# Optimization experiments

Measured on AMD Instinct MI355X. Metric: run time of the kernel, lower is better.

## Reference

```python
import jax, jax.numpy as jnp
import numpy as np

N_EMBD = 1024
HEAD_SIZE = 64
N_HEADS = 16
BLOCK_SIZE = 2048


def setup_inputs() -> dict:
    key = jax.random.key(0)
    ks = jax.random.split(key, 7)
    s = 0.02
    return {
        "X": jax.random.normal(ks[0], (2, BLOCK_SIZE, N_EMBD), dtype=jnp.float32),
        # per-head projection weights, torch Linear layout [out, in] stacked over heads
        "Wq": jax.random.normal(ks[1], (N_HEADS, HEAD_SIZE, N_EMBD), dtype=jnp.float32) * s,
        "Wk": jax.random.normal(ks[2], (N_HEADS, HEAD_SIZE, N_EMBD), dtype=jnp.float32) * s,
        "Wv": jax.random.normal(ks[3], (N_HEADS, HEAD_SIZE, N_EMBD), dtype=jnp.float32) * s,
        "Wp": jax.random.normal(ks[4], (N_EMBD, N_EMBD), dtype=jnp.float32) * s,
        "bp": jax.random.normal(ks[5], (N_EMBD,), dtype=jnp.float32) * s,
    }


def reference(X, Wq, Wk, Wv, Wp, bp):
    B, T, C = X.shape
    # per-head projections: [B,H,T,D]
    q = jnp.einsum("btc,hdc->bhtd", X, Wq)
    k = jnp.einsum("btc,hdc->bhtd", X, Wk)
    v = jnp.einsum("btc,hdc->bhtd", X, Wv)
    # NOTE: original scales by C**-0.5 where C = n_embd (not head_size)
    scores = jnp.einsum("bhtd,bhsd->bhts", q, k) * (C ** -0.5)  # [B,H,T,T]
    causal = jnp.tril(jnp.ones((T, T), dtype=bool))
    scores = jnp.where(causal, scores, -jnp.inf)
    weights = jax.nn.softmax(scores, axis=-1)
    out = jnp.einsum("bhts,bhsd->bhtd", weights, v)  # [B,H,T,D]
    # concat heads along last dim: [B,T,H*D]
    out = out.transpose(0, 2, 1, 3).reshape(B, T, -1)
    # output projection (dropout is identity in eval)
    return out @ Wp.T + bp
```

## Files before the change

kernel.cpp:

```cpp
#include <hip/hip_runtime.h>
#include <hip/hip_bf16.h>

typedef __bf16 bf16_t;
typedef __bf16 bf16x8 __attribute__((ext_vector_type(8)));
typedef __bf16 bf16x4 __attribute__((ext_vector_type(4)));
typedef float  f32x4  __attribute__((ext_vector_type(4)));
typedef unsigned int u32x4 __attribute__((ext_vector_type(4)));

#define MFMA16(a,b,c) __builtin_amdgcn_mfma_f32_16x16x32_bf16(a,b,c,0,0,0)

constexpr int B_ = 2, T_ = 2048, H_ = 16, D_ = 64, C_ = 1024;
constexpr int GK = C_;

typedef const __attribute__((address_space(1))) unsigned char ga_t;
typedef __attribute__((address_space(3))) unsigned char la_t;
__device__ __forceinline__ void gld16(const void* g, void* l) {
  __builtin_amdgcn_global_load_lds((ga_t*)g, (la_t*)l, 16, 0, 0);
}

__global__ __launch_bounds__(256) void cast_all(
    const float* __restrict__ X,  const float* __restrict__ Wq,
    const float* __restrict__ Wk, const float* __restrict__ Wv,
    const float* __restrict__ Wp,
    bf16_t* __restrict__ Xb,  bf16_t* __restrict__ Wqb, bf16_t* __restrict__ Wkb,
    bf16_t* __restrict__ Wvb, bf16_t* __restrict__ Wpb)
{
  int i = blockIdx.x * 256 + threadIdx.x;
  const float* src; bf16_t* dst; int off;
  if      (i < 1048576) { src = X;  dst = Xb;  off = i; }
  else if (i < 1310720) { src = Wq; dst = Wqb; off = i - 1048576; }
  else if (i < 1572864) { src = Wk; dst = Wkb; off = i - 1310720; }
  else if (i < 1835008) { src = Wv; dst = Wvb; off = i - 1572864; }
  else                  { src = Wp; dst = Wpb; off = i - 1835008; }
  float4 v = *reinterpret_cast<const float4*>(src + (size_t)off * 4);
  bf16x4 o;
  o[0] = (bf16_t)v.x; o[1] = (bf16_t)v.y; o[2] = (bf16_t)v.z; o[3] = (bf16_t)v.w;
  *reinterpret_cast<bf16x4*>(dst + (size_t)off * 4) = o;
}

__device__ __forceinline__ void gemm128_core(
    const bf16_t* __restrict__ A, const bf16_t* __restrict__ Bw,
    bf16_t* sA, bf16_t* sB, f32x4 (&acc)[4][2], int bx, int by)
{
  const int tid = threadIdx.x, lane = tid & 63, wid = tid >> 6;
  const int wm = wid >> 2, wn = wid & 3;
  const int g = lane >> 4, c = lane & 15, rk = c & 7;
  const int srow = tid >> 3;
  const int sg   = (tid & 7) ^ (srow & 7);
  const bf16_t* asrc = A  + (size_t)(bx * 128 + srow) * GK + sg * 8;
  const bf16_t* bsrc = Bw + (size_t)(by * 128 + srow) * GK + sg * 8;

  #define STGP(buf, kt)                                                       \
    { char* da = (char*)sA + (buf) * 16384;                                   \
      char* db = (char*)sB + (buf) * 16384;                                   \
      _Pragma("unroll")                                                       \
      for (int it = 0; it < 2; ++it) {                                        \
        gld16(asrc + (size_t)it * 65536 + (kt) * 64, da + (it * 512 + tid) * 16); \
        gld16(bsrc + (size_t)it * 65536 + (kt) * 64, db + (it * 512 + tid) * 16); \
      } }

  #define ITERP(t, buf)                                                       \
    {                                                                         \
      if ((t) < 15) asm volatile("s_waitcnt vmcnt(4)" ::: "memory");          \
      else          asm volatile("s_waitcnt vmcnt(0)" ::: "memory");          \
      __builtin_amdgcn_s_barrier();                       \
      const char* ca = (const char*)sA + (buf) * 16384;                       \
      const char* cb = (const char*)sB + (buf) * 16384;                       \
      bf16x8 af[4][2], bfr[2][2];                                             \
      _Pragma("unroll")                                                       \
      for (int mi = 0; mi < 4; ++mi)                                          \
        _Pragma("unroll")                                                     \
        for (int ks = 0; ks < 2; ++ks)                                        \
          af[mi][ks] = *reinterpret_cast<const bf16x8*>(                      \
              ca + (wm * 64 + mi * 16 + c) * 128 + (((ks * 4 + g) ^ rk) * 16)); \
      _Pragma("unroll")                                                       \
      for (int ni = 0; ni < 2; ++ni)                                          \
        _Pragma("unroll")                                                     \
        for (int ks = 0; ks < 2; ++ks)                                        \
          bfr[ni][ks] = *reinterpret_cast<const bf16x8*>(                     \
              cb + (wn * 32 + ni * 16 + c) * 128 + (((ks * 4 + g) ^ rk) * 16)); \
      asm volatile("s_waitcnt lgkmcnt(0)" ::: "memory");   \
      __builtin_amdgcn_s_barrier();                       \
      if ((t) + 2 < 16) STGP(buf, (t) + 2);          \
      __builtin_amdgcn_s_setprio(1);                                          \
      _Pragma("unroll")                                                       \
      for (int ks = 0; ks < 2; ++ks)                                          \
        _Pragma("unroll")                                                     \
        for (int mi = 0; mi < 4; ++mi)                                        \
          _Pragma("unroll")                                                   \
          for (int ni = 0; ni < 2; ++ni)                                      \
            acc[mi][ni] = MFMA16(af[mi][ks], bfr[ni][ks], acc[mi][ni]);       \
      __builtin_amdgcn_s_setprio(0);                                          \
    }

  STGP(0, 0);
  STGP(1, 1);
  #pragma unroll 1
  for (int t0 = 0; t0 < 16; t0 += 2) {
    ITERP(t0, 0);
    ITERP(t0 + 1, 1);
  }
  #undef ITERP
  #undef STGP
}

__global__ __launch_bounds__(512, 2) void gemm_qkv(
    const bf16_t* __restrict__ Xb, const bf16_t* __restrict__ Wqkv,
    bf16_t* __restrict__ qo, bf16_t* __restrict__ ko, bf16_t* __restrict__ vto)
{
  __shared__ bf16_t sA[2][128 * 64];
  __shared__ bf16_t sB[2][128 * 64];
  f32x4 acc[4][2] = {};
  const int bx = blockIdx.x, by = blockIdx.y;
  gemm128_core(Xb, Wqkv, &sA[0][0], &sB[0][0], acc, bx, by);

  const int tid = threadIdx.x, lane = tid & 63, wid = tid >> 6;
  const int wm = wid >> 2, wn = wid & 3;
  const int g = lane >> 4, c = lane & 15;
  const float qscale = 0.04508422002778f;
  const int mode = by >> 3;
  #pragma unroll
  for (int ni = 0; ni < 2; ++ni) {
    int col = by * 128 + wn * 32 + ni * 16 + c;
    int cm  = col & 1023;
    int h = cm >> 6, d = cm & 63;
    #pragma unroll
    for (int mi = 0; mi < 4; ++mi) {
      int row0 = bx * 128 + wm * 64 + mi * 16 + g * 4;
      int b = row0 >> 11, tt0 = row0 & 2047;
      if (mode == 2) {
        bf16x4 wv;
        #pragma unroll
        for (int r = 0; r < 4; ++r) wv[r] = (bf16_t)acc[mi][ni][r];
        *reinterpret_cast<bf16x4*>(
            &vto[((size_t)(b * H_ + h) * D_ + d) * T_ + tt0]) = wv;
      } else {
        bf16_t* dst = (mode == 0) ? qo : ko;
        float   sc  = (mode == 0) ? qscale : 1.0f;
        #pragma unroll
        for (int r = 0; r < 4; ++r)
          dst[((size_t)(b * H_ + h) * T_ + (tt0 + r)) * D_ + d] =
              (bf16_t)(acc[mi][ni][r] * sc);
      }
    }
  }
}

__global__ __launch_bounds__(256, 4) void attn_fwd(
    const bf16_t* __restrict__ q, const bf16_t* __restrict__ k,
    const bf16_t* __restrict__ vt, bf16_t* __restrict__ att)
{
  __shared__ bf16_t sK[2][64 * 64], sV[2][64 * 64];
  const int tid = threadIdx.x, lane = tid & 63, w = tid >> 6;
  const int g = lane >> 4, c = lane & 15;
  const int bid = blockIdx.x;
  const int qt = 31 - (bid >> 5);
  const int bh = bid & 31;
  const bf16_t* qb = q  + (size_t)bh * T_ * D_;
  const bf16_t* kb = k  + (size_t)bh * T_ * D_;
  const bf16_t* vb = vt + (size_t)bh * D_ * T_;

  bf16x8 qa[2];
  #pragma unroll
  for (int ks = 0; ks < 2; ++ks)
    qa[ks] = *reinterpret_cast<const bf16x8*>(
        qb + (size_t)(qt * 64 + w * 16 + c) * D_ + ks * 32 + g * 8);

  const int srow = tid >> 3, sgr0 = tid & 7;
  #define STAGE(buf, kt)                                                        \
    {                                                                           \
      char* kdst = (char*)sK + (size_t)(buf) * 8192;                            \
      char* vdst = (char*)sV + (size_t)(buf) * 8192;                            \
      _Pragma("unroll")                                                         \
      for (int it = 0; it < 2; ++it) {                                          \
        int idx = it * 256 + tid;                                               \
        int row = it * 32 + srow;                                               \
        int sg  = sgr0 ^ (row & 7);                                             \
        gld16(kb + (size_t)((kt) * 64 + row) * D_ + sg * 8, kdst + idx * 16);   \
        gld16(vb + (size_t)row * T_ + (kt) * 64 + sg * 8,   vdst + idx * 16);   \
      }                                                                         \
    }

  STAGE(0, 0);
  if (qt >= 1) STAGE(1, 1);

  float l_r = 0.f;
  f32x4 acc_t[4] = {};
  const int rowK = c & 7;

  #pragma unroll 1
  for (int kt = 0; kt <= qt; ++kt) {
    const int cur = kt & 1;
    if (kt < qt) asm volatile("s_waitcnt vmcnt(4)" ::: "memory");
    else         asm volatile("s_waitcnt vmcnt(0)" ::: "memory");
    __builtin_amdgcn_s_barrier();

    const char* kc = (char*)sK + (size_t)cur * 8192;
    const char* vc = (char*)sV + (size_t)cur * 8192;
    bf16x8 kf[2][4], vf[2][4];
    #pragma unroll
    for (int ks = 0; ks < 2; ++ks)
      #pragma unroll
      for (int f = 0; f < 4; ++f) {
        int rb = (f * 16 + c) * 128;
        int gsw = ((ks * 4 + g) ^ rowK) * 16;
        kf[ks][f] = *reinterpret_cast<const bf16x8*>(kc + rb + gsw);
        vf[ks][f] = *reinterpret_cast<const bf16x8*>(vc + rb + gsw);
      }
    asm volatile("s_waitcnt lgkmcnt(0)" ::: "memory");
    __builtin_amdgcn_s_barrier();
    if (kt + 2 <= qt) STAGE(cur, kt + 2);

    f32x4 s[4];
    #pragma unroll
    for (int fj = 0; fj < 4; ++fj) {
      s[fj][0] = -8.f; s[fj][1] = -8.f; s[fj][2] = -8.f; s[fj][3] = -8.f;
    }
    __builtin_amdgcn_s_setprio(1);
    #pragma unroll
    for (int fj = 0; fj < 4; ++fj)
      #pragma unroll
      for (int ks = 0; ks < 2; ++ks)
        s[fj] = MFMA16(kf[ks][fj], qa[ks], s[fj]);
    __builtin_amdgcn_s_setprio(0);

    if (kt == qt) {
      #pragma unroll
      for (int fj = 0; fj < 4; ++fj)
        #pragma unroll
        for (int r = 0; r < 4; ++r)
          if (fj * 16 + g * 4 + r > w * 16 + c) s[fj][r] = -1e30f;
    }

    unsigned pk[4][2];
    float ls[4];
    #pragma unroll
    for (int fj = 0; fj < 4; ++fj) {
      float pe0 = __builtin_amdgcn_exp2f(s[fj][0]);
      float pe1 = __builtin_amdgcn_exp2f(s[fj][1]);
      float pe2 = __builtin_amdgcn_exp2f(s[fj][2]);
      float pe3 = __builtin_amdgcn_exp2f(s[fj][3]);
      ls[fj] = (pe0 + pe1) + (pe2 + pe3);
      asm("v_cvt_pk_bf16_f32 %0, %1, %2" : "=v"(pk[fj][0]) : "v"(pe0), "v"(pe1));
      asm("v_cvt_pk_bf16_f32 %0, %1, %2" : "=v"(pk[fj][1]) : "v"(pe2), "v"(pe3));
    }
    l_r += (ls[0] + ls[1]) + (ls[2] + ls[3]);

    bf16x8 pf[2];
    #pragma unroll
    for (int ks = 0; ks < 2; ++ks) {
      unsigned x0 = pk[2 * ks][0], y0 = pk[2 * ks + 1][0];
      unsigned x1 = pk[2 * ks][1], y1 = pk[2 * ks + 1][1];
      asm("v_permlane32_swap_b32 %0, %1" : "+v"(x0), "+v"(y0));
      asm("v_permlane32_swap_b32 %0, %1" : "+v"(x1), "+v"(y1));
      asm("v_permlane16_swap_b32 %0, %1" : "+v"(x0), "+v"(y0));
      asm("v_permlane16_swap_b32 %0, %1" : "+v"(x1), "+v"(y1));
      u32x4 t; t[0] = x0; t[1] = x1; t[2] = y0; t[3] = y1;
      pf[ks] = __builtin_bit_cast(bf16x8, t);
    }

    __builtin_amdgcn_s_setprio(1);
    #pragma unroll
    for (int fd = 0; fd < 4; ++fd)
      #pragma unroll
      for (int ks = 0; ks < 2; ++ks)
        acc_t[fd] = MFMA16(vf[ks][fd], pf[ks], acc_t[fd]);
    __builtin_amdgcn_s_setprio(0);
  }

  l_r += __shfl_xor(l_r, 16);
  l_r += __shfl_xor(l_r, 32);
  float inv = 1.0f / l_r;
  const int b = bh >> 4, h = bh & 15;
  const int t = qt * 64 + w * 16 + c;
  #pragma unroll
  for (int fd = 0; fd < 4; ++fd) {
    bf16x4 wv;
    #pragma unroll
    for (int r = 0; r < 4; ++r) wv[r] = (bf16_t)(acc_t[fd][r] * inv);
    int d = fd * 16 + g * 4;
    *reinterpret_cast<bf16x4*>(&att[((size_t)(b * T_ + t) * H_ + h) * D_ + d]) = wv;
  }
  #undef STAGE
}

__global__ __launch_bounds__(512, 2) void gemm_proj(
    const bf16_t* __restrict__ attb, const bf16_t* __restrict__ Wpb,
    const float* __restrict__ bp, float* __restrict__ out)
{
  __shared__ bf16_t sA[2][128 * 64];
  __shared__ bf16_t sB[2][128 * 64];
  f32x4 acc[4][2] = {};
  const int bx = blockIdx.x, by = blockIdx.y;
  gemm128_core(attb, Wpb, &sA[0][0], &sB[0][0], acc, bx, by);

  const int tid = threadIdx.x, lane = tid & 63, wid = tid >> 6;
  const int wm = wid >> 2, wn = wid & 3;
  const int g = lane >> 4, c = lane & 15;
  #pragma unroll
  for (int m = 0; m < 4; ++m)
    #pragma unroll
    for (int n = 0; n < 2; ++n)
      #pragma unroll
      for (int r = 0; r < 4; ++r) {
        int row = bx * 128 + wm * 64 + m * 16 + g * 4 + r;
        int col = by * 128 + wn * 32 + n * 16 + c;
        out[(size_t)row * C_ + col] = acc[m][n][r] + bp[col];
      }
}

extern "C" void kernel_launch(void* const* d_in, const int* in_sizes, int n_in,
                              void* d_out, int out_size, void* d_ws, size_t ws_size,
                              hipStream_t stream)
{
  const float* X  = (const float*)d_in[0];
  const float* Wq = (const float*)d_in[1];
  const float* Wk = (const float*)d_in[2];
  const float* Wv = (const float*)d_in[3];
  const float* Wp = (const float*)d_in[4];
  const float* bp = (const float*)d_in[5];
  float* out = (float*)d_out;

  char* ws = (char*)d_ws;
  bf16_t* Xb   = (bf16_t*)(ws);
  bf16_t* Wqb  = (bf16_t*)(ws + ((size_t)8  << 20));
  bf16_t* Wkb  = (bf16_t*)(ws + ((size_t)10 << 20));
  bf16_t* Wvb  = (bf16_t*)(ws + ((size_t)12 << 20));
  bf16_t* Wpb  = (bf16_t*)(ws + ((size_t)14 << 20));
  bf16_t* qo   = (bf16_t*)(ws + ((size_t)16 << 20));
  bf16_t* ko   = (bf16_t*)(ws + ((size_t)24 << 20));
  bf16_t* vto  = (bf16_t*)(ws + ((size_t)32 << 20));
  bf16_t* attb = (bf16_t*)(ws + ((size_t)40 << 20));

  cast_all<<<8192, 256, 0, stream>>>(X, Wq, Wk, Wv, Wp, Xb, Wqb, Wkb, Wvb, Wpb);
  gemm_qkv<<<dim3(32, 24), 512, 0, stream>>>(Xb, Wqb, qo, ko, vto);
  attn_fwd<<<1024, 256, 0, stream>>>(qo, ko, vto, attb);
  gemm_proj<<<dim3(32, 8), 512, 0, stream>>>(attb, Wpb, bp, out);
}
```

Measured before the change: 88.46 us.

## Enlarge QKV GEMM tiles to 256x256 with interleaved quarter-stage loads

The QKV projection GEMM now has each 512-thread block compute a 256x256 output tile instead of 128x128, giving 8x4 MFMA accumulators per wave and a 16x12 grid. Loading of the next K-slice is split into four half-tile stages interleaved with four MFMA quadrant phases, using a 128KB double-buffered LDS with XOR swizzle. The aim is more operand reuse per byte loaded and overlap of global-to-LDS copies with compute. The cost is far more registers and LDS (occupancy likely drops to one block per CU despite launch_bounds(512,2)) and a 192-block grid that may underfill the CUs.

```diff
diff --git a/kernel.cpp b/kernel.cpp
--- a/kernel.cpp
+++ b/kernel.cpp
@@ -108,25 +108,109 @@
     const bf16_t* __restrict__ Xb, const bf16_t* __restrict__ Wqkv,
     bf16_t* __restrict__ qo, bf16_t* __restrict__ ko, bf16_t* __restrict__ vto)
 {
-  __shared__ bf16_t sA[2][128 * 64];
-  __shared__ bf16_t sB[2][128 * 64];
-  f32x4 acc[4][2] = {};
-  const int bx = blockIdx.x, by = blockIdx.y;
-  gemm128_core(Xb, Wqkv, &sA[0][0], &sB[0][0], acc, bx, by);
-
+  __shared__ bf16_t smem_[2][4][128 * 64];
+  char* smem = (char*)smem_;
   const int tid = threadIdx.x, lane = tid & 63, wid = tid >> 6;
   const int wm = wid >> 2, wn = wid & 3;
-  const int g = lane >> 4, c = lane & 15;
+  const int g = lane >> 4, c = lane & 15, rk = c & 7;
+  const int bx = blockIdx.x, by = blockIdx.y;
+  const int srow = tid >> 3;
+  const int sg   = (tid & 7) ^ (srow & 7);
+  const bf16_t* asrc = Xb   + (size_t)(bx * 256 + srow) * GK + sg * 8;
+  const bf16_t* bsrc = Wqkv + (size_t)(by * 256 + srow) * GK + sg * 8;
+  f32x4 acc[8][4] = {};
+
+  #define STG_A(h, kt)                                                        \
+    { char* d = smem + ((kt) & 1) * 65536 + (h) * 16384;                      \
+      _Pragma("unroll")                                                       \
+      for (int it = 0; it < 2; ++it)                                          \
+        gld16(asrc + (size_t)((h) * 128 + it * 64) * GK + (kt) * 64,          \
+              d + (it * 512 + tid) * 16); }
+  #define STG_B(h, kt)                                                        \
+    { char* d = smem + ((kt) & 1) * 65536 + 32768 + (h) * 16384;              \
+      _Pragma("unroll")                                                       \
+      for (int it = 0; it < 2; ++it)                                          \
+        gld16(bsrc + (size_t)((h) * 128 + it * 64) * GK + (kt) * 64,          \
+              d + (it * 512 + tid) * 16); }
+
+  #define RD_A8(lo)                                                           \
+    _Pragma("unroll")                                                         \
+    for (int i = 0; i < 4; ++i)                                               \
+      _Pragma("unroll")                                                       \
+      for (int ks = 0; ks < 2; ++ks)                                          \
+        af[i][ks] = *reinterpret_cast<const bf16x8*>(                         \
+            ca + (((lo) + i) * 16 + c) * 128 + (((ks * 4 + g) ^ rk) * 16));
+  #define RD_B4(lo)                                                           \
+    _Pragma("unroll")                                                         \
+    for (int i = 0; i < 2; ++i)                                               \
+      _Pragma("unroll")                                                       \
+      for (int ks = 0; ks < 2; ++ks)                                          \
+        bfr[(lo) + i][ks] = *reinterpret_cast<const bf16x8*>(                 \
+            cb + (bro + ((lo) + i) * 16 + c) * 128 + (((ks * 4 + g) ^ rk) * 16));
+  #define MMQ(alo, nlo)                                                       \
+    __builtin_amdgcn_s_setprio(1);                                            \
+    _Pragma("unroll")                                                         \
+    for (int ks = 0; ks < 2; ++ks)                                            \
+      _Pragma("unroll")                                                       \
+      for (int i = 0; i < 4; ++i)                                             \
+        _Pragma("unroll")                                                     \
+        for (int n = 0; n < 2; ++n)                                           \
+          acc[(alo) + i][(nlo) + n] =                                         \
+              MFMA16(af[i][ks], bfr[(nlo) + n][ks], acc[(alo) + i][(nlo) + n]); \
+    __builtin_amdgcn_s_setprio(0);
+
+  STG_A(0, 0); STG_A(1, 0); STG_B(0, 0); STG_B(1, 0);
+  STG_B(0, 1); STG_B(1, 1);
+
+  #pragma unroll 1
+  for (int t = 0; t < 16; ++t) {
+    const int cur = t & 1;
+    if (t == 15) asm volatile("s_waitcnt vmcnt(0)" ::: "memory");
+    else         asm volatile("s_waitcnt vmcnt(4)" ::: "memory");
+    __builtin_amdgcn_s_barrier();
+    const char* ca = smem + cur * 65536 + wm * 16384;
+    const char* cb = smem + cur * 65536 + 32768 + (wn >> 1) * 16384;
+    const int bro = (wn & 1) * 64;
+    bf16x8 af[4][2], bfr[4][2];
+
+    RD_A8(0) RD_B4(0)
+    if (t + 1 < 16) STG_A(0, t + 1);
+    __builtin_amdgcn_s_barrier();
+    asm volatile("s_waitcnt lgkmcnt(0)" ::: "memory");
+    MMQ(0, 0)
+    __builtin_amdgcn_s_barrier();
+    RD_B4(2)
+    if (t + 1 < 16) STG_A(1, t + 1);
+    __builtin_amdgcn_s_barrier();
+    asm volatile("s_waitcnt lgkmcnt(0)" ::: "memory");
+    MMQ(0, 2)
+    __builtin_amdgcn_s_barrier();
+    RD_A8(4)
+    if (t + 2 < 16) STG_B(0, t + 2);
+    __builtin_amdgcn_s_barrier();
+    asm volatile("s_waitcnt lgkmcnt(0)" ::: "memory");
+    MMQ(4, 2)
+    __builtin_amdgcn_s_barrier();
+    if (t + 2 < 16) STG_B(1, t + 2);
+    __builtin_amdgcn_s_barrier();
+    MMQ(4, 0)
+  }
+  #undef MMQ
+  #undef RD_B4
+  #undef RD_A8
+  #undef STG_B
+  #undef STG_A
+
   const float qscale = 0.04508422002778f;
-  const int mode = by >> 3;
+  const int mode = by >> 2;
   #pragma unroll
-  for (int ni = 0; ni < 2; ++ni) {
-    int col = by * 128 + wn * 32 + ni * 16 + c;
+  for (int ni = 0; ni < 4; ++ni) {
+    int col = by * 256 + wn * 64 + ni * 16 + c;
     int cm  = col & 1023;
     int h = cm >> 6, d = cm & 63;
     #pragma unroll
-    for (int mi = 0; mi < 4; ++mi) {
-      int row0 = bx * 128 + wm * 64 + mi * 16 + g * 4;
+    for (int mi = 0; mi < 8; ++mi) {
+      int row0 = bx * 256 + wm * 128 + mi * 16 + g * 4;
       int b = row0 >> 11, tt0 = row0 & 2047;
       if (mode == 2) {
         bf16x4 wv;
@@ -333,7 +417,7 @@
   bf16_t* attb = (bf16_t*)(ws + ((size_t)40 << 20));
 
   cast_all<<<8192, 256, 0, stream>>>(X, Wq, Wk, Wv, Wp, Xb, Wqb, Wkb, Wvb, Wpb);
-  gemm_qkv<<<dim3(32, 24), 512, 0, stream>>>(Xb, Wqb, qo, ko, vto);
+  gemm_qkv<<<dim3(16, 12), 512, 0, stream>>>(Xb, Wqb, qo, ko, vto);
   attn_fwd<<<1024, 256, 0, stream>>>(qo, ko, vto, attb);
   gemm_proj<<<dim3(32, 8), 512, 0, stream>>>(attb, Wpb, bp, out);
 }
```

Measured after the change: 93.23 us. 1.05x slower.

## Split long causal attention rows across two blocks with a reduce kernel

Applied to the files above, without the earlier changes.

Query tiles 16-31, which have the longest causal KV loops, are now split into two halves handled by separate blocks. Each half writes fp16 partial outputs and row sums to workspace, and a new attn_reduce kernel combines them. This balances work across blocks and shortens the tail of the causal attention grid. The cost is an extra kernel launch, extra global traffic for the partials, and fp16 precision on the partial accumulators. The partials rely on a fixed score offset rather than a running max, which is what lets the halves simply add. The partial buffers reuse the Xb and weight workspace regions, which are dead by this point except Wpb. lpart sits at offset 8MB (the Wqb region), so Wpb at 14MB is not overwritten.

```diff
diff --git a/kernel.cpp b/kernel.cpp
--- a/kernel.cpp
+++ b/kernel.cpp
@@ -6,6 +6,7 @@
 typedef __bf16 bf16x4 __attribute__((ext_vector_type(4)));
 typedef float  f32x4  __attribute__((ext_vector_type(4)));
 typedef unsigned int u32x4 __attribute__((ext_vector_type(4)));
+typedef _Float16 f16x4 __attribute__((ext_vector_type(4)));
 
 #define MFMA16(a,b,c) __builtin_amdgcn_mfma_f32_16x16x32_bf16(a,b,c,0,0,0)
 
@@ -148,14 +149,30 @@
 
 __global__ __launch_bounds__(256, 4) void attn_fwd(
     const bf16_t* __restrict__ q, const bf16_t* __restrict__ k,
-    const bf16_t* __restrict__ vt, bf16_t* __restrict__ att)
+    const bf16_t* __restrict__ vt, bf16_t* __restrict__ att,
+    _Float16* __restrict__ opart, float* __restrict__ lpart)
 {
   __shared__ bf16_t sK[2][64 * 64], sV[2][64 * 64];
   const int tid = threadIdx.x, lane = tid & 63, w = tid >> 6;
   const int g = lane >> 4, c = lane & 15;
   const int bid = blockIdx.x;
-  const int qt = 31 - (bid >> 5);
-  const int bh = bid & 31;
+
+  int qt, bh, k0, kE, half, tile;
+  bool split;
+  if (bid < 512) {
+    qt = 15 - (bid >> 5); bh = bid & 31;
+    k0 = 0; kE = qt; split = false; half = 0; tile = 0;
+  } else {
+    int sid = bid - 512;
+    qt = 31 - (sid >> 6);
+    int rem = sid & 63; bh = rem >> 1; half = rem & 1;
+    int sp = (qt + 1) >> 1;
+    k0 = half ? sp : 0;
+    kE = half ? qt : sp - 1;
+    split = true;
+    tile = (31 - qt) * 32 + bh;
+  }
+
   const bf16_t* qb = q  + (size_t)bh * T_ * D_;
   const bf16_t* kb = k  + (size_t)bh * T_ * D_;
   const bf16_t* vb = vt + (size_t)bh * D_ * T_;
@@ -181,17 +198,17 @@
       }                                                                         \
     }
 
-  STAGE(0, 0);
-  if (qt >= 1) STAGE(1, 1);
+  STAGE(0, k0);
+  if (k0 + 1 <= kE) STAGE(1, k0 + 1);
 
   float l_r = 0.f;
   f32x4 acc_t[4] = {};
   const int rowK = c & 7;
 
   #pragma unroll 1
-  for (int kt = 0; kt <= qt; ++kt) {
-    const int cur = kt & 1;
-    if (kt < qt) asm volatile("s_waitcnt vmcnt(4)" ::: "memory");
+  for (int kt = k0; kt <= kE; ++kt) {
+    const int cur = (kt - k0) & 1;
+    if (kt < kE) asm volatile("s_waitcnt vmcnt(4)" ::: "memory");
     else         asm volatile("s_waitcnt vmcnt(0)" ::: "memory");
     __builtin_amdgcn_s_barrier();
 
@@ -209,7 +226,7 @@
       }
     asm volatile("s_waitcnt lgkmcnt(0)" ::: "memory");
     __builtin_amdgcn_s_barrier();
-    if (kt + 2 <= qt) STAGE(cur, kt + 2);
+    if (kt + 2 <= kE) STAGE(cur, kt + 2);
 
     f32x4 s[4];
     #pragma unroll
@@ -270,18 +287,58 @@
 
   l_r += __shfl_xor(l_r, 16);
   l_r += __shfl_xor(l_r, 32);
-  float inv = 1.0f / l_r;
+
+  if (!split) {
+    float inv = 1.0f / l_r;
+    const int b = bh >> 4, h = bh & 15;
+    const int t = qt * 64 + w * 16 + c;
+    #pragma unroll
+    for (int fd = 0; fd < 4; ++fd) {
+      bf16x4 wv;
+      #pragma unroll
+      for (int r = 0; r < 4; ++r) wv[r] = (bf16_t)(acc_t[fd][r] * inv);
+      int d = fd * 16 + g * 4;
+      *reinterpret_cast<bf16x4*>(&att[((size_t)(b * T_ + t) * H_ + h) * D_ + d]) = wv;
+    }
+  } else {
+    size_t obase = ((size_t)(half * 512 + tile) * 256 + tid) * 16;
+    #pragma unroll
+    for (int fd = 0; fd < 4; ++fd) {
+      f16x4 hv;
+      #pragma unroll
+      for (int r = 0; r < 4; ++r) hv[r] = (_Float16)acc_t[fd][r];
+      *reinterpret_cast<f16x4*>(opart + obase + fd * 4) = hv;
+    }
+    if (g == 0) lpart[(half * 512 + tile) * 64 + w * 16 + c] = l_r;
+  }
+  #undef STAGE
+}
+
+__global__ __launch_bounds__(256) void attn_reduce(
+    const _Float16* __restrict__ opart, const float* __restrict__ lpart,
+    bf16_t* __restrict__ att)
+{
+  const int tile = blockIdx.x;
+  const int qt = 31 - (tile >> 5), bh = tile & 31;
+  const int tid = threadIdx.x, lane = tid & 63, w = tid >> 6;
+  const int g = lane >> 4, c = lane & 15;
+  const size_t o0 = ((size_t)tile * 256 + tid) * 16;
+  const size_t o1 = ((size_t)(512 + tile) * 256 + tid) * 16;
+  float l = lpart[tile * 64 + w * 16 + c] + lpart[(512 + tile) * 64 + w * 16 + c];
+  float inv = 1.0f / l;
   const int b = bh >> 4, h = bh & 15;
   const int t = qt * 64 + w * 16 + c;
   #pragma unroll
   for (int fd = 0; fd < 4; ++fd) {
+    f16x4 a = *reinterpret_cast<const f16x4*>(opart + o0 + fd * 4);
+    f16x4 bq = *reinterpret_cast<const f16x4*>(opart + o1 + fd * 4);
     bf16x4 wv;
     #pragma unroll
-    for (int r = 0; r < 4; ++r) wv[r] = (bf16_t)(acc_t[fd][r] * inv);
+    for (int r = 0; r < 4; ++r)
+      wv[r] = (bf16_t)(((float)a[r] + (float)bq[r]) * inv);
     int d = fd * 16 + g * 4;
     *reinterpret_cast<bf16x4*>(&att[((size_t)(b * T_ + t) * H_ + h) * D_ + d]) = wv;
   }
-  #undef STAGE
 }
 
 __global__ __launch_bounds__(512, 2) void gemm_proj(
@@ -331,9 +388,12 @@
   bf16_t* ko   = (bf16_t*)(ws + ((size_t)24 << 20));
   bf16_t* vto  = (bf16_t*)(ws + ((size_t)32 << 20));
   bf16_t* attb = (bf16_t*)(ws + ((size_t)40 << 20));
+  _Float16* opart = (_Float16*)(ws);
+  float*    lpart = (float*)(ws + ((size_t)8 << 20));
 
   cast_all<<<8192, 256, 0, stream>>>(X, Wq, Wk, Wv, Wp, Xb, Wqb, Wkb, Wvb, Wpb);
   gemm_qkv<<<dim3(32, 24), 512, 0, stream>>>(Xb, Wqb, qo, ko, vto);
-  attn_fwd<<<1024, 256, 0, stream>>>(qo, ko, vto, attb);
+  attn_fwd<<<1536, 256, 0, stream>>>(qo, ko, vto, attb, opart, lpart);
+  attn_reduce<<<512, 256, 0, stream>>>(opart, lpart, attb);
   gemm_proj<<<dim3(32, 8), 512, 0, stream>>>(attb, Wpb, bp, out);
 }
```

Measured after the change: 92.27 us. +4.3%, slower.

## Fuse Q/K/V projection tiles into one workgroup sharing the X tile

Applied to the files above, without the earlier changes.

The QKV GEMM now launches 32x8 workgroups instead of 32x24. Each workgroup loops over the three weight segments (Q, K, V) for the same X row tile, running the K-loop 48 times with a continuous double-buffered pipeline and writing an epilogue after every 16 steps. The intent is to keep the X tile hot in L2/cache across the three projections and to amortise pipeline warmup. The trade-off is three times fewer workgroups (256) on a large-CU GPU, which lowers parallelism and occupancy.

```diff
diff --git a/kernel.cpp b/kernel.cpp
--- a/kernel.cpp
+++ b/kernel.cpp
@@ -110,40 +110,113 @@
 {
   __shared__ bf16_t sA[2][128 * 64];
   __shared__ bf16_t sB[2][128 * 64];
-  f32x4 acc[4][2] = {};
-  const int bx = blockIdx.x, by = blockIdx.y;
-  gemm128_core(Xb, Wqkv, &sA[0][0], &sB[0][0], acc, bx, by);
-
   const int tid = threadIdx.x, lane = tid & 63, wid = tid >> 6;
   const int wm = wid >> 2, wn = wid & 3;
-  const int g = lane >> 4, c = lane & 15;
+  const int g = lane >> 4, c = lane & 15, rk = c & 7;
+  const int bx = blockIdx.x, by = blockIdx.y;
+  const int srow = tid >> 3;
+  const int sg   = (tid & 7) ^ (srow & 7);
+  const bf16_t* asrc = Xb   + (size_t)(bx * 128 + srow) * GK + sg * 8;
+  const bf16_t* bsrc = Wqkv + (size_t)(by * 128 + srow) * GK + sg * 8;
+  f32x4 acc[4][2] = {};
   const float qscale = 0.04508422002778f;
-  const int mode = by >> 3;
-  #pragma unroll
-  for (int ni = 0; ni < 2; ++ni) {
-    int col = by * 128 + wn * 32 + ni * 16 + c;
-    int cm  = col & 1023;
-    int h = cm >> 6, d = cm & 63;
-    #pragma unroll
-    for (int mi = 0; mi < 4; ++mi) {
-      int row0 = bx * 128 + wm * 64 + mi * 16 + g * 4;
-      int b = row0 >> 11, tt0 = row0 & 2047;
-      if (mode == 2) {
-        bf16x4 wv;
-        #pragma unroll
-        for (int r = 0; r < 4; ++r) wv[r] = (bf16_t)acc[mi][ni][r];
-        *reinterpret_cast<bf16x4*>(
-            &vto[((size_t)(b * H_ + h) * D_ + d) * T_ + tt0]) = wv;
-      } else {
-        bf16_t* dst = (mode == 0) ? qo : ko;
-        float   sc  = (mode == 0) ? qscale : 1.0f;
-        #pragma unroll
-        for (int r = 0; r < 4; ++r)
-          dst[((size_t)(b * H_ + h) * T_ + (tt0 + r)) * D_ + d] =
-              (bf16_t)(acc[mi][ni][r] * sc);
-      }
-    }
+
+  #define STGQ(buf, tt_)                                                      \
+    { int kt_ = (tt_) & 15;                                                   \
+      size_t sb_ = (size_t)((tt_) >> 4) * 1048576;                            \
+      char* da = (char*)sA + (buf) * 16384;                                   \
+      char* db = (char*)sB + (buf) * 16384;                                   \
+      _Pragma("unroll")                                                       \
+      for (int it = 0; it < 2; ++it) {                                        \
+        gld16(asrc + (size_t)it * 65536 + kt_ * 64, da + (it * 512 + tid) * 16); \
+        gld16(bsrc + sb_ + (size_t)it * 65536 + kt_ * 64, db + (it * 512 + tid) * 16); \
+      } }
+
+  #define ITERQ(tt_, buf, WAITOP)                                             \
+    {                                                                         \
+      WAITOP;                                                                 \
+      __builtin_amdgcn_s_barrier();                            \
+      const char* ca = (const char*)sA + (buf) * 16384;                       \
+      const char* cb = (const char*)sB + (buf) * 16384;                       \
+      bf16x8 af[4][2], bfr[2][2];                                             \
+      _Pragma("unroll")                                                       \
+      for (int mi = 0; mi < 4; ++mi)                                          \
+        _Pragma("unroll")                                                     \
+        for (int ks = 0; ks < 2; ++ks)                                        \
+          af[mi][ks] = *reinterpret_cast<const bf16x8*>(                      \
+              ca + (wm * 64 + mi * 16 + c) * 128 + (((ks * 4 + g) ^ rk) * 16)); \
+      _Pragma("unroll")                                                       \
+      for (int ni = 0; ni < 2; ++ni)                                          \
+        _Pragma("unroll")                                                     \
+        for (int ks = 0; ks < 2; ++ks)                                        \
+          bfr[ni][ks] = *reinterpret_cast<const bf16x8*>(                     \
+              cb + (wn * 32 + ni * 16 + c) * 128 + (((ks * 4 + g) ^ rk) * 16)); \
+      asm volatile("s_waitcnt lgkmcnt(0)" ::: "memory");   \
+      __builtin_amdgcn_s_barrier();                       \
+      if ((tt_) + 2 < 48) STGQ(buf, (tt_) + 2);      \
+      __builtin_amdgcn_s_setprio(1);                                          \
+      _Pragma("unroll")                                                       \
+      for (int ks = 0; ks < 2; ++ks)                                          \
+        _Pragma("unroll")                                                     \
+        for (int mi = 0; mi < 4; ++mi)                                        \
+          _Pragma("unroll")                                                   \
+          for (int ni = 0; ni < 2; ++ni)                                      \
+            acc[mi][ni] = MFMA16(af[mi][ks], bfr[ni][ks], acc[mi][ni]);       \
+      __builtin_amdgcn_s_setprio(0);                                          \
+    }
+
+  #define EPIQ(segv)                                                          \
+    { const int mode = (segv);                                                \
+      _Pragma("unroll")                                                       \
+      for (int ni = 0; ni < 2; ++ni) {                                        \
+        int cm = by * 128 + wn * 32 + ni * 16 + c;                            \
+        int h = cm >> 6, d = cm & 63;                                         \
+        _Pragma("unroll")                                                     \
+        for (int mi = 0; mi < 4; ++mi) {                                      \
+          int row0 = bx * 128 + wm * 64 + mi * 16 + g * 4;                    \
+          int b = row0 >> 11, tt0 = row0 & 2047;                              \
+          if (mode == 2) {                                                    \
+            bf16x4 wv;                                                        \
+            _Pragma("unroll")                                                 \
+            for (int r = 0; r < 4; ++r) wv[r] = (bf16_t)acc[mi][ni][r];       \
+            *reinterpret_cast<bf16x4*>(                                       \
+                &vto[((size_t)(b * H_ + h) * D_ + d) * T_ + tt0]) = wv;       \
+          } else {                                                            \
+            bf16_t* dst = (mode == 0) ? qo : ko;                              \
+            float   sc  = (mode == 0) ? qscale : 1.0f;                        \
+            _Pragma("unroll")                                                 \
+            for (int r = 0; r < 4; ++r)                                       \
+              dst[((size_t)(b * H_ + h) * T_ + (tt0 + r)) * D_ + d] =         \
+                  (bf16_t)(acc[mi][ni][r] * sc);                              \
+          }                                                                   \
+        }                                                                     \
+      }                                                                       \
+      _Pragma("unroll")                                                       \
+      for (int mi = 0; mi < 4; ++mi)                                          \
+        _Pragma("unroll")                                                     \
+        for (int ni = 0; ni < 2; ++ni)                                        \
+          acc[mi][ni] = (f32x4){0.f, 0.f, 0.f, 0.f};                          \
+    }
+
+  #define VM4 asm volatile("s_waitcnt vmcnt(4)" ::: "memory")
+  #define VM0 asm volatile("s_waitcnt vmcnt(0)" ::: "memory")
+
+  STGQ(0, 0);
+  STGQ(1, 1);
+  #pragma unroll 1
+  for (int t2 = 0; t2 < 46; t2 += 2) {
+    ITERQ(t2,     0, VM4);
+    ITERQ(t2 + 1, 1, VM4);
+    if ((t2 & 15) == 14) EPIQ(t2 >> 4);
   }
+  ITERQ(46, 0, VM4);
+  ITERQ(47, 1, VM0);
+  EPIQ(2);
+  #undef VM0
+  #undef VM4
+  #undef EPIQ
+  #undef ITERQ
+  #undef STGQ
 }
 
 __global__ __launch_bounds__(256, 4) void attn_fwd(
@@ -333,7 +406,7 @@
   bf16_t* attb = (bf16_t*)(ws + ((size_t)40 << 20));
 
   cast_all<<<8192, 256, 0, stream>>>(X, Wq, Wk, Wv, Wp, Xb, Wqb, Wkb, Wvb, Wpb);
-  gemm_qkv<<<dim3(32, 24), 512, 0, stream>>>(Xb, Wqb, qo, ko, vto);
+  gemm_qkv<<<dim3(32, 8), 512, 0, stream>>>(Xb, Wqb, qo, ko, vto);
   attn_fwd<<<1024, 256, 0, stream>>>(qo, ko, vto, attb);
   gemm_proj<<<dim3(32, 8), 512, 0, stream>>>(attb, Wpb, bp, out);
 }
```

Measured after the change: 93.06 us. 1.05x slower.
